# Optimization experiments

Measured on AMD Instinct MI355X. Metric: run time of the kernel, lower is better.

## Reference

```python
import jax, jax.numpy as jnp
import numpy as np

N, E, G = 100000, 400000, 2000
F_IN, HID, H = 74, 64, 4
HID4 = HID * H           # 256, per-node feature after flatten(1)
POOL = 3 * HID4          # 768, concat(mean, max, sum)
OUT = 128
NEG_SLOPE = 0.2          # DGL GATConv default LeakyReLU slope


def setup_inputs() -> dict:
    key = jax.random.key(0)
    ks = jax.random.split(key, 20)
    p = lambda k, shape: (jax.random.normal(k, shape, jnp.float32) * 0.05)
    inp = {
        "node_feat": jax.random.normal(ks[0], (N, F_IN), jnp.float32),
        "src": jax.random.randint(ks[1], (E,), 0, N, jnp.int32),
        "dst": jax.random.randint(ks[2], (E,), 0, N, jnp.int32),
        # every graph gets exactly N//G nodes (sorted, non-empty segments)
        "graph_ids": jnp.arange(N, dtype=jnp.int32) // (N // G),
        "enc_W": p(ks[3], (F_IN, HID)), "enc_b": jnp.zeros((HID,), jnp.float32),
    }
    in_dims = [HID, HID4, HID4]
    for l in range(3):
        inp[f"W{l}"] = p(ks[4 + 4 * l], (in_dims[l], H * HID))
        inp[f"al{l}"] = p(ks[5 + 4 * l], (H, HID))
        inp[f"ar{l}"] = p(ks[6 + 4 * l], (H, HID))
        inp[f"b{l}"] = jnp.zeros((H * HID,), jnp.float32)
    inp["r1_W"] = p(ks[16], (POOL, HID)); inp["r1_b"] = jnp.zeros((HID,), jnp.float32)
    inp["r2_W"] = p(ks[17], (HID, OUT)); inp["r2_b"] = jnp.zeros((OUT,), jnp.float32)
    return inp


def _gat_layer(h, src, dst, W, al, ar, b):
    # DGL GATConv (eval mode: dropouts are identity), activation=ReLU
    z = (h @ W).reshape(N, H, HID)                       # [N,H,O]
    el = jnp.einsum("nho,ho->nh", z, al)                 # [N,H]
    er = jnp.einsum("nho,ho->nh", z, ar)
    e = jax.nn.leaky_relu(el[src] + er[dst], NEG_SLOPE)  # [E,H]
    # segment softmax over incoming edges of each dst node, per head
    m = jax.ops.segment_max(e, dst, num_segments=N)      # [N,H]
    ex = jnp.exp(e - m[dst])
    s = jax.ops.segment_sum(ex, dst, num_segments=N)     # [N,H]
    a = ex / s[dst]                                      # [E,H]
    out = jax.ops.segment_sum(z[src] * a[:, :, None], dst, num_segments=N)
    out = out + b.reshape(1, H, HID)                     # GATConv bias
    return jax.nn.relu(out).reshape(N, HID4)             # flatten(1)


def reference(node_feat, src, dst, graph_ids, enc_W, enc_b,
              W0, al0, ar0, b0, W1, al1, ar1, b1, W2, al2, ar2, b2,
              r1_W, r1_b, r2_W, r2_b):
    h = node_feat @ enc_W + enc_b                        # node encoder
    h = _gat_layer(h, src, dst, W0, al0, ar0, b0)
    h = _gat_layer(h, src, dst, W1, al1, ar1, b1)
    h = _gat_layer(h, src, dst, W2, al2, ar2, b2)
    # multi-pool readout: mean / max / sum over nodes of each graph
    h_sum = jax.ops.segment_sum(h, graph_ids, num_segments=G)
    cnt = jax.ops.segment_sum(jnp.ones((N, 1), h.dtype), graph_ids, num_segments=G)
    h_mean = h_sum / cnt
    h_max = jax.ops.segment_max(h, graph_ids, num_segments=G)
    hg = jnp.concatenate([h_mean, h_max, h_sum], axis=1)  # [G, 3*HID4]
    hg = jax.nn.relu(hg @ r1_W + r1_b)
    return hg @ r2_W + r2_b                              # [G, OUT]
```

## Files before the change

kernel.cpp:

```cpp
#include <hip/hip_runtime.h>

#define N_NODES 100000
#define N_EDGES 400000
#define N_GRAPHS 2000
#define F_IN 74
#define ENC_KP 96
#define HID 64
#define NHEAD 4
#define HID4 256
#define OUT_DIM 128
#define NODES_PER_G 50

typedef __attribute__((ext_vector_type(8))) short short8;
typedef __attribute__((ext_vector_type(4))) float f32x4;

__device__ inline ushort f2bf(float f) {
  union { float f; unsigned u; } v; v.f = f;
  unsigned u = v.u;
  return (ushort)((u + 0x7FFFu + ((u >> 16) & 1u)) >> 16);
}
__device__ inline float bf2f(ushort b) {
  union { unsigned u; float f; } v; v.u = ((unsigned)b) << 16;
  return v.f;
}
__device__ inline float leaky(float x) { return x >= 0.f ? x : 0.2f * x; }

__device__ inline void glds16(const ushort* g, ushort* l) {
  __builtin_amdgcn_global_load_lds(
      (const __attribute__((address_space(1))) void*)g,
      (__attribute__((address_space(3))) void*)l, 16, 0, 0);
}

__global__ __launch_bounds__(256) void k_count(const int* __restrict__ dst,
                                               int* __restrict__ off) {
  int e = blockIdx.x * 256 + threadIdx.x;
  if (e < N_EDGES) atomicAdd(&off[dst[e] + 1], 1);
}

__global__ __launch_bounds__(256) void k_scan1(int* __restrict__ data, int n,
                                               int* __restrict__ blksum) {
  __shared__ int sh[256];
  int t = threadIdx.x;
  int base = blockIdx.x * 1024 + t * 4;
  int v0 = (base + 0 < n) ? data[base + 0] : 0;
  int v1 = (base + 1 < n) ? data[base + 1] : 0;
  int v2 = (base + 2 < n) ? data[base + 2] : 0;
  int v3 = (base + 3 < n) ? data[base + 3] : 0;
  v1 += v0; v2 += v1; v3 += v2;
  int tot = v3;
  sh[t] = tot;
  __syncthreads();
  for (int o = 1; o < 256; o <<= 1) {
    int x = (t >= o) ? sh[t - o] : 0;
    __syncthreads();
    sh[t] += x;
    __syncthreads();
  }
  int excl = sh[t] - tot;
  if (base + 0 < n) data[base + 0] = v0 + excl;
  if (base + 1 < n) data[base + 1] = v1 + excl;
  if (base + 2 < n) data[base + 2] = v2 + excl;
  if (base + 3 < n) data[base + 3] = v3 + excl;
  if (t == 255) blksum[blockIdx.x] = sh[255];
}

__global__ __launch_bounds__(256) void k_scan2(int* __restrict__ blksum, int nb) {
  __shared__ int sh[256];
  int t = threadIdx.x;
  sh[t] = (t < nb) ? blksum[t] : 0;
  __syncthreads();
  for (int o = 1; o < 256; o <<= 1) {
    int x = (t >= o) ? sh[t - o] : 0;
    __syncthreads();
    sh[t] += x;
    __syncthreads();
  }
  if (t < nb) blksum[t] = sh[t];
}

__global__ __launch_bounds__(256) void k_scan3(int* __restrict__ data, int n,
                                               const int* __restrict__ blksum) {
  int b = blockIdx.x;
  if (b == 0) return;
  int add = blksum[b - 1];
  int base = b * 1024 + threadIdx.x * 4;
  for (int j = 0; j < 4; ++j)
    if (base + j < n) data[base + j] += add;
}

__global__ __launch_bounds__(256) void k_scatter(const int* __restrict__ dst,
                                                 const int* __restrict__ src,
                                                 const int* __restrict__ off,
                                                 int* __restrict__ cursor,
                                                 int* __restrict__ srcs) {
  int e = blockIdx.x * 256 + threadIdx.x;
  if (e >= N_EDGES) return;
  int d = dst[e];
  int pos = off[d] + atomicAdd(&cursor[d], 1);
  srcs[pos] = src[e];
}

__global__ __launch_bounds__(256) void k_sortseg(const int* __restrict__ off,
                                                 int* __restrict__ srcs) {
  int n = blockIdx.x * 256 + threadIdx.x;
  if (n >= N_NODES) return;
  int beg = off[n], end = off[n + 1];
  for (int i = beg + 1; i < end; ++i) {
    int key = srcs[i];
    int j = i - 1;
    while (j >= beg && srcs[j] > key) { srcs[j + 1] = srcs[j]; --j; }
    srcs[j + 1] = key;
  }
}

__global__ __launch_bounds__(256) void k_wt_enc(const float* __restrict__ W,
                                                ushort* __restrict__ Wte) {
  int idx = blockIdx.x * 256 + threadIdx.x;
  if (idx >= HID * ENC_KP) return;
  int col = idx / ENC_KP;
  int k = idx - col * ENC_KP;
  ushort v = 0;
  if (k < F_IN) v = f2bf(W[(size_t)k * HID + col]);
  Wte[idx] = v;
}

__global__ __launch_bounds__(256) void k_enc_mfma(const float* __restrict__ nf,
                                                  const ushort* __restrict__ Bt,
                                                  const float* __restrict__ bias,
                                                  ushort* __restrict__ Cb) {
  __shared__ ushort As[128][104];
  __shared__ ushort Bs[64][104];
  int t = threadIdx.x;
  int lane = t & 63;
  int wid = t >> 6;
  int brow = blockIdx.x * 128;

  for (int i = t; i < 128 * ENC_KP; i += 256) {
    int r = i / ENC_KP;
    int c = i - r * ENC_KP;
    int gr = brow + r;
    float v = 0.f;
    if (gr < N_NODES && c < F_IN) v = nf[(size_t)gr * F_IN + c];
    As[r][c] = f2bf(v);
  }
  if (t < 128) {
    int r = t >> 1;
    int o = (t & 1) * 48;
#pragma unroll
    for (int i = 0; i < 6; ++i)
      *(int4*)&Bs[r][o + i * 8] = *(const int4*)(Bt + (size_t)r * ENC_KP + o + i * 8);
  }
  __syncthreads();

  int fr = lane & 15;
  int ko = (lane >> 4) * 8;
  f32x4 acc[2][4];
#pragma unroll
  for (int m = 0; m < 2; ++m)
#pragma unroll
    for (int n = 0; n < 4; ++n) acc[m][n] = (f32x4)(0.f);

#pragma unroll
  for (int ks = 0; ks < 3; ++ks) {
    short8 a[2], b[4];
#pragma unroll
    for (int m = 0; m < 2; ++m) a[m] = *(const short8*)&As[wid * 32 + m * 16 + fr][ks * 32 + ko];
#pragma unroll
    for (int n = 0; n < 4; ++n) b[n] = *(const short8*)&Bs[n * 16 + fr][ks * 32 + ko];
#pragma unroll
    for (int m = 0; m < 2; ++m)
#pragma unroll
      for (int n = 0; n < 4; ++n)
        acc[m][n] = __builtin_amdgcn_mfma_f32_16x16x32_bf16(a[m], b[n], acc[m][n], 0, 0, 0);
  }

  int r0 = (lane >> 4) * 4;
  int cc = lane & 15;
#pragma unroll
  for (int m = 0; m < 2; ++m) {
#pragma unroll
    for (int j = 0; j < 4; ++j) {
      int row = brow + wid * 32 + m * 16 + r0 + j;
      if (row >= N_NODES) continue;
#pragma unroll
      for (int n = 0; n < 4; ++n) {
        int col = n * 16 + cc;
        Cb[(size_t)row * HID + col] = f2bf(acc[m][n][j] + bias[col]);
      }
    }
  }
}

template <int K>
__global__ __launch_bounds__(256) void k_wt(const float* __restrict__ W,
                                            ushort* __restrict__ Wt) {
  int idx = blockIdx.x * 256 + threadIdx.x;
  if (idx >= K * HID4) return;
  int k = idx >> 8;
  int n = idx & 255;
  Wt[(size_t)n * K + k] = f2bf(W[idx]);
}

template <int K>
__global__ __launch_bounds__(256) void k_gemm_mfma(const ushort* __restrict__ A,
                                                   const ushort* __restrict__ Bt,
                                                   ushort* __restrict__ Cb,
                                                   const float* __restrict__ al,
                                                   const float* __restrict__ ar,
                                                   float* __restrict__ el,
                                                   float* __restrict__ er,
                                                   int n_rows) {
  __shared__ __align__(16) ushort As[2][128 * 32];
  __shared__ __align__(16) ushort Bs[2][128 * 32];
  int t = threadIdx.x;
  int lane = t & 63;
  int wid = t >> 6;
  int wr = wid >> 1, wc = wid & 1;
  int brow = blockIdx.x * 128;
  int bcol = blockIdx.y * 128;

  f32x4 acc[4][4];
#pragma unroll
  for (int m = 0; m < 4; ++m)
#pragma unroll
    for (int n = 0; n < 4; ++n) acc[m][n] = (f32x4)(0.f);

  int srow0 = (wid * 2 + 0) * 16 + (lane >> 2);
  int srow1 = (wid * 2 + 1) * 16 + (lane >> 2);
  int skc = (lane & 3) * 8;
  int ga0 = brow + srow0; if (ga0 > n_rows - 1) ga0 = n_rows - 1;
  int ga1 = brow + srow1; if (ga1 > n_rows - 1) ga1 = n_rows - 1;
  const ushort* pa0 = A + (size_t)ga0 * K + skc;
  const ushort* pa1 = A + (size_t)ga1 * K + skc;
  const ushort* pb0 = Bt + (size_t)(bcol + srow0) * K + skc;
  const ushort* pb1 = Bt + (size_t)(bcol + srow1) * K + skc;
  int lo0 = (wid * 2 + 0) * 512;
  int lo1 = (wid * 2 + 1) * 512;

  int fr = lane & 15;
  int ko = (lane >> 4) * 8;

  glds16(pa0, &As[0][lo0]);
  glds16(pa1, &As[0][lo1]);
  glds16(pb0, &Bs[0][lo0]);
  glds16(pb1, &Bs[0][lo1]);
  __syncthreads();
  int cur = 0;

  for (int k0 = 0; k0 < K; k0 += 32) {
    if (k0 + 32 < K) {
      glds16(pa0 + k0 + 32, &As[cur ^ 1][lo0]);
      glds16(pa1 + k0 + 32, &As[cur ^ 1][lo1]);
      glds16(pb0 + k0 + 32, &Bs[cur ^ 1][lo0]);
      glds16(pb1 + k0 + 32, &Bs[cur ^ 1][lo1]);
    }
    short8 a[4], b[4];
#pragma unroll
    for (int m = 0; m < 4; ++m)
      a[m] = *(const short8*)(&As[cur][0] + (wr * 64 + m * 16 + fr) * 32 + ko);
#pragma unroll
    for (int n = 0; n < 4; ++n)
      b[n] = *(const short8*)(&Bs[cur][0] + (wc * 64 + n * 16 + fr) * 32 + ko);
#pragma unroll
    for (int m = 0; m < 4; ++m)
#pragma unroll
      for (int n = 0; n < 4; ++n)
        acc[m][n] = __builtin_amdgcn_mfma_f32_16x16x32_bf16(a[m], b[n], acc[m][n], 0, 0, 0);
    __syncthreads();
    cur ^= 1;
  }

  int r0 = (lane >> 4) * 4;
  int cc = lane & 15;
  int q = blockIdx.y * 2 + wc;
  float alr[4], arr[4];
#pragma unroll
  for (int n = 0; n < 4; ++n) {
    int col = bcol + wc * 64 + n * 16 + cc;
    alr[n] = al[col];
    arr[n] = ar[col];
  }
#pragma unroll
  for (int m = 0; m < 4; ++m) {
#pragma unroll
    for (int j = 0; j < 4; ++j) {
      float pl = 0.f, pr = 0.f;
#pragma unroll
      for (int n = 0; n < 4; ++n) {
        pl = fmaf(acc[m][n][j], alr[n], pl);
        pr = fmaf(acc[m][n][j], arr[n], pr);
      }
#pragma unroll
      for (int o = 1; o < 16; o <<= 1) {
        pl += __shfl_xor(pl, o, 64);
        pr += __shfl_xor(pr, o, 64);
      }
      int row = brow + wr * 64 + m * 16 + r0 + j;
      if (row >= n_rows) continue;
      if (cc == 0) {
        el[(size_t)row * NHEAD + q] = pl;
        er[(size_t)row * NHEAD + q] = pr;
      }
#pragma unroll
      for (int n = 0; n < 4; ++n)
        Cb[(size_t)row * HID4 + bcol + wc * 64 + n * 16 + cc] = f2bf(acc[m][n][j]);
    }
  }
}

__global__ __launch_bounds__(256) void k_agg(const ushort* __restrict__ zb,
                                             const float* __restrict__ el,
                                             const float* __restrict__ er,
                                             const int* __restrict__ off,
                                             const int* __restrict__ srcs,
                                             const float* __restrict__ bias,
                                             ushort* __restrict__ outb) {
  int w = (blockIdx.x * 256 + threadIdx.x) >> 6;
  int lane = threadIdx.x & 63;
  int n = w * 4 + (lane >> 4);
  int li = lane & 15;
  if (n >= N_NODES) return;
  int h = li >> 2;
  int c = li * 16;
  int beg = off[n], end = off[n + 1];
  float erh = er[(size_t)n * NHEAD + h];

  float s = 0.f;
  float acc[16];
#pragma unroll
  for (int j = 0; j < 16; ++j) acc[j] = 0.f;

  float e0 = 0.f, e1 = 0.f, e2 = 0.f;
  int4 za0 = make_int4(0, 0, 0, 0), zb0 = za0;
  int4 za1 = za0, zb1 = za0, za2 = za0, zb2 = za0;
  if (beg < end) {
    int sn = srcs[beg];
    e0 = el[(size_t)sn * NHEAD + h];
    const ushort* zp = zb + (size_t)sn * HID4 + c;
    za0 = *(const int4*)zp; zb0 = *(const int4*)(zp + 8);
  }
  if (beg + 1 < end) {
    int sn = srcs[beg + 1];
    e1 = el[(size_t)sn * NHEAD + h];
    const ushort* zp = zb + (size_t)sn * HID4 + c;
    za1 = *(const int4*)zp; zb1 = *(const int4*)(zp + 8);
  }
  if (beg + 2 < end) {
    int sn = srcs[beg + 2];
    e2 = el[(size_t)sn * NHEAD + h];
    const ushort* zp = zb + (size_t)sn * HID4 + c;
    za2 = *(const int4*)zp; zb2 = *(const int4*)(zp + 8);
  }

  for (int p = beg; p < end; ++p) {
    float ev = e0;
    int4 va = za0, vb = zb0;
    e0 = e1; za0 = za1; zb0 = zb1;
    e1 = e2; za1 = za2; zb1 = zb2;
    if (p + 3 < end) {
      int sn = srcs[p + 3];
      e2 = el[(size_t)sn * NHEAD + h];
      const ushort* zp = zb + (size_t)sn * HID4 + c;
      za2 = *(const int4*)zp; zb2 = *(const int4*)(zp + 8);
    }
    float pv = __expf(leaky(ev + erh));
    s += pv;
    const ushort* ua = (const ushort*)&va;
    const ushort* ub = (const ushort*)&vb;
#pragma unroll
    for (int j = 0; j < 8; ++j) acc[j] = fmaf(pv, bf2f(ua[j]), acc[j]);
#pragma unroll
    for (int j = 0; j < 8; ++j) acc[8 + j] = fmaf(pv, bf2f(ub[j]), acc[8 + j]);
  }
  float inv = (s > 0.f) ? 1.f / s : 0.f;
  float bb[16];
#pragma unroll
  for (int j = 0; j < 16; j += 4) {
    float4 b4 = *(const float4*)(bias + c + j);
    bb[j] = b4.x; bb[j + 1] = b4.y; bb[j + 2] = b4.z; bb[j + 3] = b4.w;
  }
  int4 ov0, ov1;
  ushort* os0 = (ushort*)&ov0;
  ushort* os1 = (ushort*)&ov1;
#pragma unroll
  for (int j = 0; j < 8; ++j) os0[j] = f2bf(fmaxf(acc[j] * inv + bb[j], 0.f));
#pragma unroll
  for (int j = 0; j < 8; ++j) os1[j] = f2bf(fmaxf(acc[8 + j] * inv + bb[8 + j], 0.f));
  ushort* op = outb + (size_t)n * HID4 + c;
  *(int4*)op = ov0;
  *(int4*)(op + 8) = ov1;
}

__global__ __launch_bounds__(256) void k_pool_mlp(const ushort* __restrict__ h,
                                                  const float* __restrict__ r1W,
                                                  const float* __restrict__ r1b,
                                                  const float* __restrict__ r2W,
                                                  const float* __restrict__ r2b,
                                                  float* __restrict__ out) {
  __shared__ float pooled[3 * HID4];
  __shared__ float part[4][HID];
  __shared__ float mid[HID];
  int g = blockIdx.x;
  int t = threadIdx.x;
  const ushort* base = h + (size_t)g * NODES_PER_G * HID4;
  float sum = 0.f, mx = -1e30f;
  for (int i = 0; i < NODES_PER_G; ++i) {
    float v = bf2f(base[(size_t)i * HID4 + t]);
    sum += v;
    mx = fmaxf(mx, v);
  }
  pooled[t] = sum / (float)NODES_PER_G;
  pooled[HID4 + t] = mx;
  pooled[2 * HID4 + t] = sum;
  __syncthreads();
  {
    int o = t & 63, chunk = t >> 6;
    float acc = 0.f;
    int k0 = chunk * 192;
    for (int k = k0; k < k0 + 192; ++k) acc = fmaf(pooled[k], r1W[k * HID + o], acc);
    part[chunk][o] = acc;
  }
  __syncthreads();
  if (t < HID) {
    float acc = r1b[t] + part[0][t] + part[1][t] + part[2][t] + part[3][t];
    mid[t] = fmaxf(acc, 0.f);
  }
  __syncthreads();
  if (t < OUT_DIM) {
    float acc = r2b[t];
    for (int k = 0; k < HID; ++k) acc = fmaf(mid[k], r2W[k * OUT_DIM + t], acc);
    out[(size_t)g * OUT_DIM + t] = acc;
  }
}

extern "C" void kernel_launch(void* const* d_in, const int* in_sizes, int n_in,
                              void* d_out, int out_size, void* d_ws, size_t ws_size,
                              hipStream_t stream) {
  const float* node_feat = (const float*)d_in[0];
  const int* src = (const int*)d_in[1];
  const int* dst = (const int*)d_in[2];
  const float* enc_W = (const float*)d_in[4];
  const float* enc_b = (const float*)d_in[5];
  const float* Wl[3] = {(const float*)d_in[6], (const float*)d_in[10], (const float*)d_in[14]};
  const float* all[3] = {(const float*)d_in[7], (const float*)d_in[11], (const float*)d_in[15]};
  const float* arl[3] = {(const float*)d_in[8], (const float*)d_in[12], (const float*)d_in[16]};
  const float* bl[3] = {(const float*)d_in[9], (const float*)d_in[13], (const float*)d_in[17]};
  const float* r1W = (const float*)d_in[18];
  const float* r1b = (const float*)d_in[19];
  const float* r2W = (const float*)d_in[20];
  const float* r2b = (const float*)d_in[21];
  float* out = (float*)d_out;

  char* p = (char*)d_ws;
  auto alloc = [&](size_t bytes) {
    void* r = (void*)p;
    p += (bytes + 255) & ~(size_t)255;
    return r;
  };
  int* off = (int*)alloc((N_NODES + 1) * sizeof(int));
  int* cursor = (int*)alloc(N_NODES * sizeof(int));
  int* srcs = (int*)alloc(N_EDGES * sizeof(int));
  int* blksum = (int*)alloc(256 * sizeof(int));
  float* el = (float*)alloc((size_t)N_NODES * NHEAD * sizeof(float));
  float* er = (float*)alloc((size_t)N_NODES * NHEAD * sizeof(float));
  ushort* Qb = (ushort*)alloc((size_t)N_NODES * HID4 * sizeof(ushort));
  ushort* Pb = (ushort*)alloc((size_t)N_NODES * HID4 * sizeof(ushort));
  ushort* Wt = (ushort*)alloc((size_t)HID4 * HID4 * sizeof(ushort));
  ushort* Wte = (ushort*)alloc((size_t)HID * ENC_KP * sizeof(ushort));

  hipMemsetAsync(off, 0, (N_NODES + 1) * sizeof(int), stream);
  hipMemsetAsync(cursor, 0, N_NODES * sizeof(int), stream);
  k_count<<<(N_EDGES + 255) / 256, 256, 0, stream>>>(dst, off);
  const int SCAN_N = N_NODES + 1;
  const int NB = (SCAN_N + 1023) / 1024;
  k_scan1<<<NB, 256, 0, stream>>>(off, SCAN_N, blksum);
  k_scan2<<<1, 256, 0, stream>>>(blksum, NB);
  k_scan3<<<NB, 256, 0, stream>>>(off, SCAN_N, blksum);
  k_scatter<<<(N_EDGES + 255) / 256, 256, 0, stream>>>(dst, src, off, cursor, srcs);
  k_sortseg<<<(N_NODES + 255) / 256, 256, 0, stream>>>(off, srcs);

  k_wt_enc<<<(HID * ENC_KP + 255) / 256, 256, 0, stream>>>(enc_W, Wte);
  k_enc_mfma<<<(N_NODES + 127) / 128, 256, 0, stream>>>(node_feat, Wte, enc_b, Pb);

  dim3 ggrid((N_NODES + 127) / 128, HID4 / 128);
  const int AGG_BLOCKS = ((N_NODES + 3) / 4 + 3) / 4;
  for (int l = 0; l < 3; ++l) {
    if (l == 0) {
      k_wt<HID><<<(HID * HID4 + 255) / 256, 256, 0, stream>>>(Wl[0], Wt);
      k_gemm_mfma<HID><<<ggrid, 256, 0, stream>>>(Pb, Wt, Qb, all[0], arl[0], el, er, N_NODES);
    } else {
      k_wt<HID4><<<(HID4 * HID4 + 255) / 256, 256, 0, stream>>>(Wl[l], Wt);
      k_gemm_mfma<HID4><<<ggrid, 256, 0, stream>>>(Pb, Wt, Qb, all[l], arl[l], el, er, N_NODES);
    }
    k_agg<<<AGG_BLOCKS, 256, 0, stream>>>(Qb, el, er, off, srcs, bl[l], Pb);
  }

  k_pool_mlp<<<N_GRAPHS, 256, 0, stream>>>(Pb, r1W, r1b, r2W, r2b, out);
}
```

Measured before the change: 379.6 us.

## Sort nodes by in-degree for aggregation and swizzle GEMM block order

Builds a degree histogram and counting-sort permutation of nodes so each aggregation wavefront handles nodes of similar in-degree. This is meant to reduce divergence and idle lanes in the 16-lane-per-node edge loops. The GEMM grid is flattened and remapped so the two column blocks of a row panel run next to each other, aiming at better cache reuse of the A rows. The cost is three extra small kernels, and output writes in k_agg become scattered rather than sequential.

```diff
diff --git a/kernel.cpp b/kernel.cpp
--- a/kernel.cpp
+++ b/kernel.cpp
@@ -10,6 +10,7 @@
 #define HID4 256
 #define OUT_DIM 128
 #define NODES_PER_G 50
+#define DEG_BINS 64
 
 typedef __attribute__((ext_vector_type(8))) short short8;
 typedef __attribute__((ext_vector_type(4))) float f32x4;
@@ -113,6 +114,42 @@
   }
 }
 
+__global__ __launch_bounds__(256) void k_hist(const int* __restrict__ off,
+                                              int* __restrict__ hist) {
+  int n = blockIdx.x * 256 + threadIdx.x;
+  if (n >= N_NODES) return;
+  int d = off[n + 1] - off[n];
+  if (d > DEG_BINS - 1) d = DEG_BINS - 1;
+  atomicAdd(&hist[d], 1);
+}
+
+__global__ __launch_bounds__(64) void k_histscan(int* __restrict__ hist) {
+  __shared__ int sh[DEG_BINS];
+  int t = threadIdx.x;
+  int v = hist[t];
+  sh[t] = v;
+  __syncthreads();
+  for (int o = 1; o < DEG_BINS; o <<= 1) {
+    int x = (t >= o) ? sh[t - o] : 0;
+    __syncthreads();
+    sh[t] += x;
+    __syncthreads();
+  }
+  hist[t] = sh[t] - v;
+}
+
+__global__ __launch_bounds__(256) void k_order(const int* __restrict__ off,
+                                               const int* __restrict__ hist,
+                                               int* __restrict__ cur,
+                                               int* __restrict__ nord) {
+  int n = blockIdx.x * 256 + threadIdx.x;
+  if (n >= N_NODES) return;
+  int d = off[n + 1] - off[n];
+  if (d > DEG_BINS - 1) d = DEG_BINS - 1;
+  int pos = hist[d] + atomicAdd(&cur[d], 1);
+  nord[pos] = n;
+}
+
 __global__ __launch_bounds__(256) void k_wt_enc(const float* __restrict__ W,
                                                 ushort* __restrict__ Wte) {
   int idx = blockIdx.x * 256 + threadIdx.x;
@@ -212,12 +249,17 @@
                                                    int n_rows) {
   __shared__ __align__(16) ushort As[2][128 * 32];
   __shared__ __align__(16) ushort Bs[2][128 * 32];
+  int bid = blockIdx.x;
+  int rpan = (bid >> 4) * 8 + (bid & 7);
+  int nrp = (n_rows + 127) / 128;
+  if (rpan >= nrp) return;
+  int brow = rpan * 128;
+  int bcol = ((bid >> 3) & 1) * 128;
+
   int t = threadIdx.x;
   int lane = t & 63;
   int wid = t >> 6;
   int wr = wid >> 1, wc = wid & 1;
-  int brow = blockIdx.x * 128;
-  int bcol = blockIdx.y * 128;
 
   f32x4 acc[4][4];
 #pragma unroll
@@ -272,7 +314,7 @@
 
   int r0 = (lane >> 4) * 4;
   int cc = lane & 15;
-  int q = blockIdx.y * 2 + wc;
+  int q = (bcol >> 6) + wc;
   float alr[4], arr[4];
 #pragma unroll
   for (int n = 0; n < 4; ++n) {
@@ -313,13 +355,15 @@
                                              const float* __restrict__ er,
                                              const int* __restrict__ off,
                                              const int* __restrict__ srcs,
+                                             const int* __restrict__ nord,
                                              const float* __restrict__ bias,
                                              ushort* __restrict__ outb) {
   int w = (blockIdx.x * 256 + threadIdx.x) >> 6;
   int lane = threadIdx.x & 63;
-  int n = w * 4 + (lane >> 4);
+  int slot = w * 4 + (lane >> 4);
   int li = lane & 15;
-  if (n >= N_NODES) return;
+  if (slot >= N_NODES) return;
+  int n = nord[slot];
   int h = li >> 2;
   int c = li * 16;
   int beg = off[n], end = off[n + 1];
@@ -461,6 +505,9 @@
   int* cursor = (int*)alloc(N_NODES * sizeof(int));
   int* srcs = (int*)alloc(N_EDGES * sizeof(int));
   int* blksum = (int*)alloc(256 * sizeof(int));
+  int* hist = (int*)alloc(DEG_BINS * sizeof(int));
+  int* hcur = (int*)alloc(DEG_BINS * sizeof(int));
+  int* nord = (int*)alloc(N_NODES * sizeof(int));
   float* el = (float*)alloc((size_t)N_NODES * NHEAD * sizeof(float));
   float* er = (float*)alloc((size_t)N_NODES * NHEAD * sizeof(float));
   ushort* Qb = (ushort*)alloc((size_t)N_NODES * HID4 * sizeof(ushort));
@@ -470,6 +517,8 @@
 
   hipMemsetAsync(off, 0, (N_NODES + 1) * sizeof(int), stream);
   hipMemsetAsync(cursor, 0, N_NODES * sizeof(int), stream);
+  hipMemsetAsync(hist, 0, DEG_BINS * sizeof(int), stream);
+  hipMemsetAsync(hcur, 0, DEG_BINS * sizeof(int), stream);
   k_count<<<(N_EDGES + 255) / 256, 256, 0, stream>>>(dst, off);
   const int SCAN_N = N_NODES + 1;
   const int NB = (SCAN_N + 1023) / 1024;
@@ -479,20 +528,25 @@
   k_scatter<<<(N_EDGES + 255) / 256, 256, 0, stream>>>(dst, src, off, cursor, srcs);
   k_sortseg<<<(N_NODES + 255) / 256, 256, 0, stream>>>(off, srcs);
 
+  k_hist<<<(N_NODES + 255) / 256, 256, 0, stream>>>(off, hist);
+  k_histscan<<<1, DEG_BINS, 0, stream>>>(hist);
+  k_order<<<(N_NODES + 255) / 256, 256, 0, stream>>>(off, hist, hcur, nord);
+
   k_wt_enc<<<(HID * ENC_KP + 255) / 256, 256, 0, stream>>>(enc_W, Wte);
   k_enc_mfma<<<(N_NODES + 127) / 128, 256, 0, stream>>>(node_feat, Wte, enc_b, Pb);
 
-  dim3 ggrid((N_NODES + 127) / 128, HID4 / 128);
+  const int NRP = (N_NODES + 127) / 128;
+  const int GEMM_BLOCKS = ((NRP + 7) / 8) * 16;
   const int AGG_BLOCKS = ((N_NODES + 3) / 4 + 3) / 4;
   for (int l = 0; l < 3; ++l) {
     if (l == 0) {
       k_wt<HID><<<(HID * HID4 + 255) / 256, 256, 0, stream>>>(Wl[0], Wt);
-      k_gemm_mfma<HID><<<ggrid, 256, 0, stream>>>(Pb, Wt, Qb, all[0], arl[0], el, er, N_NODES);
+      k_gemm_mfma<HID><<<GEMM_BLOCKS, 256, 0, stream>>>(Pb, Wt, Qb, all[0], arl[0], el, er, N_NODES);
     } else {
       k_wt<HID4><<<(HID4 * HID4 + 255) / 256, 256, 0, stream>>>(Wl[l], Wt);
-      k_gemm_mfma<HID4><<<ggrid, 256, 0, stream>>>(Pb, Wt, Qb, all[l], arl[l], el, er, N_NODES);
+      k_gemm_mfma<HID4><<<GEMM_BLOCKS, 256, 0, stream>>>(Pb, Wt, Qb, all[l], arl[l], el, er, N_NODES);
     }
-    k_agg<<<AGG_BLOCKS, 256, 0, stream>>>(Qb, el, er, off, srcs, bl[l], Pb);
+    k_agg<<<AGG_BLOCKS, 256, 0, stream>>>(Qb, el, er, off, srcs, nord, bl[l], Pb);
   }
 
   k_pool_mlp<<<N_GRAPHS, 256, 0, stream>>>(Pb, r1W, r1b, r2W, r2b, out);
```

Result: slower. 1.199 ms (+215.8%).

## Fold attention vectors into weights, merge weight prep, swizzle GEMM grid

Applied to the files above, without the earlier changes.

Precomputes W·al and W·ar (per head) as an extra 16-column bf16 matrix in a single merged prep kernel that also transposes all layer weights at once. The GEMM then computes el/er with extra MFMAs on one wave per block instead of shuffle reductions over fp32 accumulators. It also fully unrolls the K loop and remaps the 1D grid so pairs of column tiles of the same row panel run close together for A reuse in cache. Risks: el/er now come from bf16-rounded folded weights and bf16 inputs, a small precision change, and the lr MFMAs load imbalance onto one wave.

```diff
diff --git a/kernel.cpp b/kernel.cpp
--- a/kernel.cpp
+++ b/kernel.cpp
@@ -113,15 +113,66 @@
   }
 }
 
-__global__ __launch_bounds__(256) void k_wt_enc(const float* __restrict__ W,
-                                                ushort* __restrict__ Wte) {
+__global__ __launch_bounds__(256) void k_prep(
+    const float* __restrict__ enc_W,
+    const float* __restrict__ W0, const float* __restrict__ W1,
+    const float* __restrict__ W2,
+    const float* __restrict__ al0, const float* __restrict__ ar0,
+    const float* __restrict__ al1, const float* __restrict__ ar1,
+    const float* __restrict__ al2, const float* __restrict__ ar2,
+    ushort* __restrict__ Wte,
+    ushort* __restrict__ Wt0, ushort* __restrict__ Wt1,
+    ushort* __restrict__ Wt2,
+    ushort* __restrict__ Wlr0, ushort* __restrict__ Wlr1,
+    ushort* __restrict__ Wlr2) {
+  const int S0 = HID * ENC_KP;
+  const int S1 = S0 + HID * HID4;
+  const int S2 = S1 + HID4 * HID4;
+  const int S3 = S2 + HID4 * HID4;
+  const int S4 = S3 + 16 * HID;
+  const int S5 = S4 + 16 * HID4;
+  const int S6 = S5 + 16 * HID4;
   int idx = blockIdx.x * 256 + threadIdx.x;
-  if (idx >= HID * ENC_KP) return;
-  int col = idx / ENC_KP;
-  int k = idx - col * ENC_KP;
-  ushort v = 0;
-  if (k < F_IN) v = f2bf(W[(size_t)k * HID + col]);
-  Wte[idx] = v;
+  if (idx < S0) {
+    int col = idx / ENC_KP, k = idx - col * ENC_KP;
+    Wte[idx] = (k < F_IN) ? f2bf(enc_W[(size_t)k * HID + col]) : (ushort)0;
+  } else if (idx < S1) {
+    int i = idx - S0; int k = i >> 8, n = i & 255;
+    Wt0[(size_t)n * HID + k] = f2bf(W0[i]);
+  } else if (idx < S2) {
+    int i = idx - S1; int k = i >> 8, n = i & 255;
+    Wt1[(size_t)n * HID4 + k] = f2bf(W1[i]);
+  } else if (idx < S3) {
+    int i = idx - S2; int k = i >> 8, n = i & 255;
+    Wt2[(size_t)n * HID4 + k] = f2bf(W2[i]);
+  } else if (idx < S4) {
+    int i = idx - S3; int c = i / HID, k = i - c * HID;
+    float acc = 0.f;
+    if (c < 8) {
+      const float* av = (c < 4) ? al0 + (c & 3) * 64 : ar0 + (c & 3) * 64;
+      const float* wp = W0 + (size_t)k * HID4 + (c & 3) * 64;
+      for (int o = 0; o < 64; ++o) acc = fmaf(wp[o], av[o], acc);
+    }
+    Wlr0[(size_t)c * HID + k] = f2bf(acc);
+  } else if (idx < S5) {
+    int i = idx - S4; int c = i / HID4, k = i - c * HID4;
+    float acc = 0.f;
+    if (c < 8) {
+      const float* av = (c < 4) ? al1 + (c & 3) * 64 : ar1 + (c & 3) * 64;
+      const float* wp = W1 + (size_t)k * HID4 + (c & 3) * 64;
+      for (int o = 0; o < 64; ++o) acc = fmaf(wp[o], av[o], acc);
+    }
+    Wlr1[(size_t)c * HID4 + k] = f2bf(acc);
+  } else if (idx < S6) {
+    int i = idx - S5; int c = i / HID4, k = i - c * HID4;
+    float acc = 0.f;
+    if (c < 8) {
+      const float* av = (c < 4) ? al2 + (c & 3) * 64 : ar2 + (c & 3) * 64;
+      const float* wp = W2 + (size_t)k * HID4 + (c & 3) * 64;
+      for (int o = 0; o < 64; ++o) acc = fmaf(wp[o], av[o], acc);
+    }
+    Wlr2[(size_t)c * HID4 + k] = f2bf(acc);
+  }
 }
 
 __global__ __launch_bounds__(256) void k_enc_mfma(const float* __restrict__ nf,
@@ -192,32 +243,26 @@
 }
 
 template <int K>
-__global__ __launch_bounds__(256) void k_wt(const float* __restrict__ W,
-                                            ushort* __restrict__ Wt) {
-  int idx = blockIdx.x * 256 + threadIdx.x;
-  if (idx >= K * HID4) return;
-  int k = idx >> 8;
-  int n = idx & 255;
-  Wt[(size_t)n * K + k] = f2bf(W[idx]);
-}
-
-template <int K>
 __global__ __launch_bounds__(256) void k_gemm_mfma(const ushort* __restrict__ A,
                                                    const ushort* __restrict__ Bt,
+                                                   const ushort* __restrict__ Wlr,
                                                    ushort* __restrict__ Cb,
-                                                   const float* __restrict__ al,
-                                                   const float* __restrict__ ar,
                                                    float* __restrict__ el,
                                                    float* __restrict__ er,
                                                    int n_rows) {
   __shared__ __align__(16) ushort As[2][128 * 32];
   __shared__ __align__(16) ushort Bs[2][128 * 32];
+  int bid = blockIdx.x;
+  int rpan = (bid >> 4) * 8 + (bid & 7);
+  int nrp = (n_rows + 127) / 128;
+  if (rpan >= nrp) return;
+  int brow = rpan * 128;
+  int bcol = ((bid >> 3) & 1) * 128;
+
   int t = threadIdx.x;
   int lane = t & 63;
   int wid = t >> 6;
   int wr = wid >> 1, wc = wid & 1;
-  int brow = blockIdx.x * 128;
-  int bcol = blockIdx.y * 128;
 
   f32x4 acc[4][4];
 #pragma unroll
@@ -240,14 +285,27 @@
   int fr = lane & 15;
   int ko = (lane >> 4) * 8;
 
+  bool do_lr = (bcol == 0) && (wc == 0);
+  short8 blrr[K / 32];
+  f32x4 acc_lr[4];
+#pragma unroll
+  for (int m = 0; m < 4; ++m) acc_lr[m] = (f32x4)(0.f);
+  if (do_lr) {
+#pragma unroll
+    for (int ks = 0; ks < K / 32; ++ks)
+      blrr[ks] = *(const short8*)(Wlr + (size_t)fr * K + ks * 32 + ko);
+  }
+
   glds16(pa0, &As[0][lo0]);
   glds16(pa1, &As[0][lo1]);
   glds16(pb0, &Bs[0][lo0]);
   glds16(pb1, &Bs[0][lo1]);
   __syncthreads();
-  int cur = 0;
-
-  for (int k0 = 0; k0 < K; k0 += 32) {
+
+#pragma unroll
+  for (int kstep = 0; kstep < K / 32; ++kstep) {
+    int k0 = kstep * 32;
+    int cur = kstep & 1;
     if (k0 + 32 < K) {
       glds16(pa0 + k0 + 32, &As[cur ^ 1][lo0]);
       glds16(pa1 + k0 + 32, &As[cur ^ 1][lo1]);
@@ -266,45 +324,38 @@
 #pragma unroll
       for (int n = 0; n < 4; ++n)
         acc[m][n] = __builtin_amdgcn_mfma_f32_16x16x32_bf16(a[m], b[n], acc[m][n], 0, 0, 0);
+    if (do_lr) {
+#pragma unroll
+      for (int m = 0; m < 4; ++m)
+        acc_lr[m] = __builtin_amdgcn_mfma_f32_16x16x32_bf16(a[m], blrr[kstep], acc_lr[m], 0, 0, 0);
+    }
     __syncthreads();
-    cur ^= 1;
   }
 
   int r0 = (lane >> 4) * 4;
   int cc = lane & 15;
-  int q = blockIdx.y * 2 + wc;
-  float alr[4], arr[4];
-#pragma unroll
-  for (int n = 0; n < 4; ++n) {
-    int col = bcol + wc * 64 + n * 16 + cc;
-    alr[n] = al[col];
-    arr[n] = ar[col];
-  }
 #pragma unroll
   for (int m = 0; m < 4; ++m) {
 #pragma unroll
     for (int j = 0; j < 4; ++j) {
-      float pl = 0.f, pr = 0.f;
-#pragma unroll
-      for (int n = 0; n < 4; ++n) {
-        pl = fmaf(acc[m][n][j], alr[n], pl);
-        pr = fmaf(acc[m][n][j], arr[n], pr);
-      }
-#pragma unroll
-      for (int o = 1; o < 16; o <<= 1) {
-        pl += __shfl_xor(pl, o, 64);
-        pr += __shfl_xor(pr, o, 64);
-      }
       int row = brow + wr * 64 + m * 16 + r0 + j;
       if (row >= n_rows) continue;
-      if (cc == 0) {
-        el[(size_t)row * NHEAD + q] = pl;
-        er[(size_t)row * NHEAD + q] = pr;
-      }
 #pragma unroll
       for (int n = 0; n < 4; ++n)
         Cb[(size_t)row * HID4 + bcol + wc * 64 + n * 16 + cc] = f2bf(acc[m][n][j]);
     }
+  }
+  if (do_lr && cc < 8) {
+#pragma unroll
+    for (int m = 0; m < 4; ++m)
+#pragma unroll
+      for (int j = 0; j < 4; ++j) {
+        int row = brow + wr * 64 + m * 16 + r0 + j;
+        if (row >= n_rows) continue;
+        float v = acc_lr[m][j];
+        if (cc < 4) el[(size_t)row * NHEAD + cc] = v;
+        else er[(size_t)row * NHEAD + (cc - 4)] = v;
+      }
   }
 }
 
@@ -442,7 +493,7 @@
   const float* enc_W = (const float*)d_in[4];
   const float* enc_b = (const float*)d_in[5];
   const float* Wl[3] = {(const float*)d_in[6], (const float*)d_in[10], (const float*)d_in[14]};
-  const float* all[3] = {(const float*)d_in[7], (const float*)d_in[11], (const float*)d_in[15]};
+  const float* all_[3] = {(const float*)d_in[7], (const float*)d_in[11], (const float*)d_in[15]};
   const float* arl[3] = {(const float*)d_in[8], (const float*)d_in[12], (const float*)d_in[16]};
   const float* bl[3] = {(const float*)d_in[9], (const float*)d_in[13], (const float*)d_in[17]};
   const float* r1W = (const float*)d_in[18];
@@ -465,8 +516,13 @@
   float* er = (float*)alloc((size_t)N_NODES * NHEAD * sizeof(float));
   ushort* Qb = (ushort*)alloc((size_t)N_NODES * HID4 * sizeof(ushort));
   ushort* Pb = (ushort*)alloc((size_t)N_NODES * HID4 * sizeof(ushort));
-  ushort* Wt = (ushort*)alloc((size_t)HID4 * HID4 * sizeof(ushort));
   ushort* Wte = (ushort*)alloc((size_t)HID * ENC_KP * sizeof(ushort));
+  ushort* Wt0 = (ushort*)alloc((size_t)HID4 * HID * sizeof(ushort));
+  ushort* Wt1 = (ushort*)alloc((size_t)HID4 * HID4 * sizeof(ushort));
+  ushort* Wt2 = (ushort*)alloc((size_t)HID4 * HID4 * sizeof(ushort));
+  ushort* Wlr0 = (ushort*)alloc((size_t)16 * HID * sizeof(ushort));
+  ushort* Wlr1 = (ushort*)alloc((size_t)16 * HID4 * sizeof(ushort));
+  ushort* Wlr2 = (ushort*)alloc((size_t)16 * HID4 * sizeof(ushort));
 
   hipMemsetAsync(off, 0, (N_NODES + 1) * sizeof(int), stream);
   hipMemsetAsync(cursor, 0, N_NODES * sizeof(int), stream);
@@ -479,19 +535,24 @@
   k_scatter<<<(N_EDGES + 255) / 256, 256, 0, stream>>>(dst, src, off, cursor, srcs);
   k_sortseg<<<(N_NODES + 255) / 256, 256, 0, stream>>>(off, srcs);
 
-  k_wt_enc<<<(HID * ENC_KP + 255) / 256, 256, 0, stream>>>(enc_W, Wte);
+  const int PREP_N = HID * ENC_KP + HID * HID4 + 2 * HID4 * HID4 +
+                     16 * (HID + HID4 + HID4);
+  k_prep<<<(PREP_N + 255) / 256, 256, 0, stream>>>(
+      enc_W, Wl[0], Wl[1], Wl[2], all_[0], arl[0], all_[1], arl[1], all_[2], arl[2],
+      Wte, Wt0, Wt1, Wt2, Wlr0, Wlr1, Wlr2);
+
   k_enc_mfma<<<(N_NODES + 127) / 128, 256, 0, stream>>>(node_feat, Wte, enc_b, Pb);
 
-  dim3 ggrid((N_NODES + 127) / 128, HID4 / 128);
+  const int NRP = (N_NODES + 127) / 128;
+  const int GEMM_BLOCKS = ((NRP + 7) / 8) * 16;
   const int AGG_BLOCKS = ((N_NODES + 3) / 4 + 3) / 4;
+  const ushort* Wts[3] = {Wt0, Wt1, Wt2};
+  const ushort* Wlrs[3] = {Wlr0, Wlr1, Wlr2};
   for (int l = 0; l < 3; ++l) {
-    if (l == 0) {
-      k_wt<HID><<<(HID * HID4 + 255) / 256, 256, 0, stream>>>(Wl[0], Wt);
-      k_gemm_mfma<HID><<<ggrid, 256, 0, stream>>>(Pb, Wt, Qb, all[0], arl[0], el, er, N_NODES);
-    } else {
-      k_wt<HID4><<<(HID4 * HID4 + 255) / 256, 256, 0, stream>>>(Wl[l], Wt);
-      k_gemm_mfma<HID4><<<ggrid, 256, 0, stream>>>(Pb, Wt, Qb, all[l], arl[l], el, er, N_NODES);
-    }
+    if (l == 0)
+      k_gemm_mfma<HID><<<GEMM_BLOCKS, 256, 0, stream>>>(Pb, Wts[0], Wlrs[0], Qb, el, er, N_NODES);
+    else
+      k_gemm_mfma<HID4><<<GEMM_BLOCKS, 256, 0, stream>>>(Pb, Wts[l], Wlrs[l], Qb, el, er, N_NODES);
     k_agg<<<AGG_BLOCKS, 256, 0, stream>>>(Qb, el, er, off, srcs, bl[l], Pb);
   }
 
```

Result: faster. 355.9 us (-6.2%).
